# Optimization experiments

Measured on AMD Instinct MI355X. Metric: run time of the kernel, lower is better.

## Reference

```python
import jax, jax.numpy as jnp
import numpy as np
import math

B, S, E, H = 2, 2048, 1024, 16
D = E // H
EPS = 1e-5


def setup_inputs() -> dict:
    key = jax.random.key(0)
    ks = jax.random.split(key, 6)
    s = 1.0 / math.sqrt(E)
    return {
        "query": jax.random.normal(ks[0], (B, S, E), jnp.float32),
        "Wq": jax.random.normal(ks[1], (E, E), jnp.float32) * s,
        "bq": jnp.zeros((E,), jnp.float32),
        "Wk": jax.random.normal(ks[2], (E, E), jnp.float32) * s,
        "bk": jnp.zeros((E,), jnp.float32),
        "Wv": jax.random.normal(ks[3], (E, E), jnp.float32) * s,
        "bv": jnp.zeros((E,), jnp.float32),
        "Wo": jax.random.normal(ks[4], (E, E), jnp.float32) * s,
        "bo": jnp.zeros((E,), jnp.float32),
        "alpha": jnp.ones((1,), jnp.float32),
    }


def reference(query, Wq, bq, Wk, bk, Wv, bv, Wo, bo, alpha):
    # Q/K/V projections (nn.Linear: x @ W.T + b)
    q = (query @ Wq.T + bq).reshape(B, S, H, D)
    k = (query @ Wk.T + bk).reshape(B, S, H, D)
    v = (query @ Wv.T + bv).reshape(B, S, H, D)

    # YAT scores: (q.k)^2 / (||q-k||^2 + eps)
    qk = jnp.einsum('bqhd,bkhd->bhqk', q, k)          # [B,H,S,S]
    sq = jnp.einsum('bqhd,bqhd->bhq', q, q)           # ||q||^2
    sk = jnp.einsum('bkhd,bkhd->bhk', k, k)           # ||k||^2
    dist_sq = sq[..., :, None] + sk[..., None, :] - 2.0 * qk
    scores = (qk * qk) / (dist_sq + EPS)

    # learnable alpha scaling: scores * (sqrt(d)/log(1+d))^alpha
    scale = (jnp.sqrt(jnp.float32(D)) / jnp.log1p(jnp.float32(D))) ** alpha[0]
    scores = scores * scale

    attn = jax.nn.softmax(scores, axis=-1)
    out = jnp.einsum('bhqk,bkhd->bqhd', attn, v).reshape(B, S, E)
    return out @ Wo.T + bo
```

## Files before the change

kernel.cpp:

```cpp
#include <hip/hip_runtime.h>
#include <hip/hip_fp16.h>
#include <math.h>

#define BB 2
#define SS 2048
#define EE 1024
#define HH 16
#define DD 64
#define YAT_EPS 1e-5f
#define RR (BB * HH * SS)

typedef __attribute__((ext_vector_type(8))) short bf16x8;
typedef __attribute__((ext_vector_type(4))) short short4v;
typedef __attribute__((ext_vector_type(4))) float f32x4;
#define MFMA16(a, b, c) __builtin_amdgcn_mfma_f32_16x16x32_bf16((a), (b), (c), 0, 0, 0)

#if __has_builtin(__builtin_amdgcn_exp2f)
#define EXP2(x) __builtin_amdgcn_exp2f(x)
#else
#define EXP2(x) exp2f(x)
#endif
#if __has_builtin(__builtin_amdgcn_rcpf)
#define RCPF(x) __builtin_amdgcn_rcpf(x)
#else
#define RCPF(x) (1.0f / (x))
#endif

__device__ __forceinline__ unsigned short f2bf(float x) {
    unsigned int u = __float_as_uint(x);
    u += 0x7FFFu + ((u >> 16) & 1u);
    return (unsigned short)(u >> 16);
}
__device__ __forceinline__ float bf2f(unsigned short h) {
    return __uint_as_float(((unsigned int)h) << 16);
}
__device__ __forceinline__ short f2bf_t(float x) {
    return (short)(__float_as_uint(x) >> 16);
}

__device__ __forceinline__ void async_ld16(void* lds, const void* g) {
    __builtin_amdgcn_global_load_lds(
        (const __attribute__((address_space(1))) unsigned int*)g,
        (__attribute__((address_space(3))) unsigned int*)lds, 16, 0, 0);
}

__global__ __launch_bounds__(256) void split_f32(const float* __restrict__ in,
                                                 unsigned short* __restrict__ hi,
                                                 unsigned short* __restrict__ lo,
                                                 int n4) {
    int i = blockIdx.x * 256 + threadIdx.x;
    if (i >= n4) return;
    float4 v = ((const float4*)in)[i];
    ushort4 h, l;
    h.x = f2bf(v.x); l.x = f2bf(v.x - bf2f(h.x));
    h.y = f2bf(v.y); l.y = f2bf(v.y - bf2f(h.y));
    h.z = f2bf(v.z); l.z = f2bf(v.z - bf2f(h.z));
    h.w = f2bf(v.w); l.w = f2bf(v.w - bf2f(h.w));
    ((ushort4*)hi)[i] = h;
    ((ushort4*)lo)[i] = l;
}

__global__ __launch_bounds__(256) void split_w4(
        const float* __restrict__ Wq, const float* __restrict__ Wk,
        const float* __restrict__ Wv, const float* __restrict__ Wo,
        unsigned short* __restrict__ Whi, unsigned short* __restrict__ Wlo,
        unsigned short* __restrict__ Wohi) {
    int i = blockIdx.x * 256 + threadIdx.x;
    int y = blockIdx.y;
    const float* src = y == 0 ? Wq : y == 1 ? Wk : y == 2 ? Wv : Wo;
    unsigned short* hi = y < 3 ? Whi + (size_t)y * EE * EE : Wohi;
    float4 v = ((const float4*)src)[i];
    ushort4 h;
    h.x = f2bf(v.x); h.y = f2bf(v.y); h.z = f2bf(v.z); h.w = f2bf(v.w);
    ((ushort4*)hi)[i] = h;
    if (y < 2) {
        unsigned short* lo = Wlo + (size_t)y * EE * EE;
        ushort4 l;
        l.x = f2bf(v.x - bf2f(h.x));
        l.y = f2bf(v.y - bf2f(h.y));
        l.z = f2bf(v.z - bf2f(h.z));
        l.w = f2bf(v.w - bf2f(h.w));
        ((ushort4*)lo)[i] = l;
    }
}

template <int MODE, int PASSES>
__global__ __launch_bounds__(256, 2) void gemm3p(
        const unsigned short* __restrict__ Ahi, const unsigned short* __restrict__ Alo,
        const unsigned short* __restrict__ Bhi, const unsigned short* __restrict__ Blo,
        const float* __restrict__ bq, const float* __restrict__ bk,
        const float* __restrict__ bv,
        float* __restrict__ Cf,
        unsigned short* __restrict__ qhi, unsigned short* __restrict__ qlo,
        unsigned short* __restrict__ khi,
        unsigned short* __restrict__ v_sd,
        float* __restrict__ sqn, float* __restrict__ skn,
        int M, int N, int K) {
    __shared__ __align__(16) unsigned short LA_hi[128 * 32];
    __shared__ __align__(16) unsigned short LA_lo[128 * 32];
    __shared__ __align__(16) unsigned short LB_hi[128 * 32];
    __shared__ __align__(16) unsigned short LB_lo[128 * 32];

    const int t = threadIdx.x;
    const int w = t >> 6, lane = t & 63;
    const int quad = lane >> 4, lr = lane & 15;
    const int wy = w & 1, wx = w >> 1;
    const int m0 = blockIdx.y * 128, n0 = blockIdx.x * 128;

    const unsigned short* gsrc = nullptr;
    unsigned short* ldst = nullptr;
    if (w == 0)      { gsrc = Ahi + (size_t)m0 * K; ldst = LA_hi; }
    else if (w == 2) { gsrc = Bhi + (size_t)n0 * K; ldst = LB_hi; }
    else if (PASSES == 3 && w == 1) { gsrc = Alo + (size_t)m0 * K; ldst = LA_lo; }
    else if (PASSES == 3 && w == 3) { gsrc = Blo + (size_t)n0 * K; ldst = LB_lo; }
    const unsigned short* gl = gsrc ? gsrc + (size_t)(lane >> 2) * K + (lane & 3) * 8
                                    : nullptr;

    f32x4 acc[4][4];
    #pragma unroll
    for (int i = 0; i < 4; ++i)
        #pragma unroll
        for (int j = 0; j < 4; ++j)
            acc[i][j] = (f32x4){0.f, 0.f, 0.f, 0.f};

    for (int k0 = 0; k0 < K; k0 += 32) {
        __syncthreads();
        if (gl) {
            #pragma unroll
            for (int i = 0; i < 8; ++i)
                async_ld16(ldst + i * 512, gl + (size_t)i * 16 * K + k0);
        }
        __syncthreads();
        bf16x8 ah[4], al[4], bh_[4], bl_[4];
        #pragma unroll
        for (int i = 0; i < 4; ++i) {
            ah[i]  = *(const bf16x8*)&LA_hi[(wy * 64 + i * 16 + lr) * 32 + quad * 8];
            bh_[i] = *(const bf16x8*)&LB_hi[(wx * 64 + i * 16 + lr) * 32 + quad * 8];
            if (PASSES == 3) {
                al[i]  = *(const bf16x8*)&LA_lo[(wy * 64 + i * 16 + lr) * 32 + quad * 8];
                bl_[i] = *(const bf16x8*)&LB_lo[(wx * 64 + i * 16 + lr) * 32 + quad * 8];
            }
        }
        #pragma unroll
        for (int mg = 0; mg < 4; ++mg)
            #pragma unroll
            for (int ns = 0; ns < 4; ++ns) {
                f32x4 a = acc[mg][ns];
                a = MFMA16(ah[mg], bh_[ns], a);
                if (PASSES == 3) {
                    a = MFMA16(ah[mg], bl_[ns], a);
                    a = MFMA16(al[mg], bh_[ns], a);
                }
                acc[mg][ns] = a;
            }
    }

    const int ng = n0 + wx * 64;
    if (MODE == 0) {
        float bias_v[4];
        #pragma unroll
        for (int ns = 0; ns < 4; ++ns) bias_v[ns] = bq[ng + ns * 16 + lr];
        #pragma unroll
        for (int mg = 0; mg < 4; ++mg)
            #pragma unroll
            for (int r = 0; r < 4; ++r) {
                int m = m0 + wy * 64 + mg * 16 + quad * 4 + r;
                #pragma unroll
                for (int ns = 0; ns < 4; ++ns)
                    Cf[(size_t)m * N + ng + ns * 16 + lr] = acc[mg][ns][r] + bias_v[ns];
            }
    } else {
        const int path = MODE == 1 ? (ng >> 10) : 2;
        const int c = MODE == 1 ? (ng & 1023) : ng;
        const int h = c >> 6;
        const float* bias = path == 0 ? bq : path == 1 ? bk : bv;
        unsigned short* hi_p = path == 0 ? qhi : path == 1 ? khi : v_sd;
        float* nrm = path == 0 ? sqn : skn;
        float bias_v[4];
        #pragma unroll
        for (int ns = 0; ns < 4; ++ns) bias_v[ns] = bias[c + ns * 16 + lr];
        #pragma unroll
        for (int mg = 0; mg < 4; ++mg)
            #pragma unroll
            for (int r = 0; r < 4; ++r) {
                int m = m0 + wy * 64 + mg * 16 + quad * 4 + r;
                int b = m >> 11, s = m & (SS - 1);
                size_t base = ((size_t)(b * HH + h) * SS + s) * DD;
                float v4[4];
                #pragma unroll
                for (int ns = 0; ns < 4; ++ns) v4[ns] = acc[mg][ns][r] + bias_v[ns];
                if (path < 2) {
                    float pn = v4[0] * v4[0] + v4[1] * v4[1] + v4[2] * v4[2] + v4[3] * v4[3];
                    #pragma unroll
                    for (int off = 1; off < 16; off <<= 1) pn += __shfl_xor(pn, off);
                    if (lr == 0) nrm[(size_t)(b * HH + h) * SS + s] = pn;
                    #pragma unroll
                    for (int ns = 0; ns < 4; ++ns) {
                        unsigned short hv = f2bf(v4[ns]);
                        hi_p[base + ns * 16 + lr] = hv;
                        if (path == 0)
                            qlo[base + ns * 16 + lr] = f2bf(v4[ns] - bf2f(hv));
                    }
                } else {
                    #pragma unroll
                    for (int ns = 0; ns < 4; ++ns)
                        hi_p[base + ns * 16 + lr] = f2bf(v4[ns]);
                }
            }
    }
}

__global__ __launch_bounds__(256) void transpose_v(const unsigned short* __restrict__ v_sd,
                                                   unsigned short* __restrict__ vt) {
    __shared__ unsigned short T[64][65];
    const int t = threadIdx.x;
    const int bh = blockIdx.y, s0 = blockIdx.x * 64;
    {
        int sl = t >> 2, d4 = (t & 3) * 16;
        const unsigned short* src = &v_sd[((size_t)bh * SS + s0 + sl) * DD + d4];
        bf16x8 a = *(const bf16x8*)src;
        bf16x8 b = *(const bf16x8*)(src + 8);
        #pragma unroll
        for (int j = 0; j < 8; ++j) {
            T[sl][d4 + j] = (unsigned short)a[j];
            T[sl][d4 + 8 + j] = (unsigned short)b[j];
        }
    }
    __syncthreads();
    {
        int dl = t >> 2, s4 = (t & 3) * 16;
        bf16x8 a, b;
        #pragma unroll
        for (int j = 0; j < 8; ++j) {
            a[j] = (short)T[s4 + j][dl];
            b[j] = (short)T[s4 + 8 + j][dl];
        }
        unsigned short* dst = &vt[((size_t)bh * DD + dl) * SS + s0 + s4];
        *(bf16x8*)dst = a;
        *(bf16x8*)(dst + 8) = b;
    }
}

__global__ __launch_bounds__(256, 3) void yat_attn_mfma(
        const unsigned short* __restrict__ qhi, const unsigned short* __restrict__ qlo,
        const unsigned short* __restrict__ khi,
        const unsigned short* __restrict__ vt,
        const float* __restrict__ sqn, const float* __restrict__ skn,
        const float* __restrict__ alphap,
        __half* __restrict__ Opart, float2* __restrict__ mlpart) {
    __shared__ __align__(16) unsigned short Ks[2][8192];
    __shared__ __align__(16) unsigned short Ps[2][4][16 * 68];

    const int t = threadIdx.x;
    const int w = t >> 6, lane = t & 63;
    const int quad = lane >> 4, lr = lane & 15;
    const int qt = blockIdx.x, bh = blockIdx.y, z = blockIdx.z;
    const int row0 = qt * 64 + w * 16;
    const float cscale = powf(sqrtf((float)DD) / log1pf((float)DD), alphap[0])
                         * 1.4426950408889634f;

    bf16x8 qh[2], ql[2];
    #pragma unroll
    for (int kd = 0; kd < 2; ++kd) {
        size_t o = ((size_t)bh * SS + row0 + lr) * DD + kd * 32 + quad * 8;
        qh[kd] = *(const bf16x8*)&qhi[o];
        ql[kd] = *(const bf16x8*)&qlo[o];
    }
    const float sqe = sqn[(size_t)bh * SS + row0 + lr] + YAT_EPS;

    const int lrow = lane >> 3;
    const int lofs = lrow * 64 + (((lane & 7) ^ (lrow & 7)) << 3);
    const int sw = lr & 7;

    float m_r = -INFINITY, l_r = 0.f;
    f32x4 O[4];
    #pragma unroll
    for (int nd = 0; nd < 4; ++nd) O[nd] = (f32x4){0.f, 0.f, 0.f, 0.f};

    const int t0 = z * 16;
    const size_t khi_base = (size_t)bh * SS * 64 + (size_t)w * 16 * 64 + lofs;
    const size_t skn_base = (size_t)bh * SS + quad * 4;

    #pragma unroll
    for (int tl = 0; tl < 2; ++tl)
        #pragma unroll
        for (int i2 = 0; i2 < 2; ++i2)
            async_ld16(&Ks[0][tl * 4096 + w * 1024 + i2 * 512],
                       khi + khi_base + (size_t)(t0 + tl) * 4096 + i2 * 512);

    for (int it = 0; it < 8; ++it) {
        const int p = it & 1;
        __syncthreads();
        if (it + 1 < 8) {
            #pragma unroll
            for (int tl = 0; tl < 2; ++tl)
                #pragma unroll
                for (int i2 = 0; i2 < 2; ++i2)
                    async_ld16(&Ks[p ^ 1][tl * 4096 + w * 1024 + i2 * 512],
                               khi + khi_base
                                   + (size_t)(t0 + 2 * (it + 1) + tl) * 4096
                                   + i2 * 512);
        }
        #pragma unroll
        for (int sub = 0; sub < 2; ++sub) {
            const int kbase = (t0 + 2 * it + sub) * 64;
            const unsigned short* kb = &Ks[p][sub * 4096];
            f32x4 acc[4];
            f32x4 sk4[4];
            #pragma unroll
            for (int st = 0; st < 4; ++st) {
                const int rbase = (st * 16 + lr) * 64;
                bf16x8 kh0 = *(const bf16x8*)&kb[rbase + ((quad    ) ^ sw) * 8];
                bf16x8 kh1 = *(const bf16x8*)&kb[rbase + ((quad + 4) ^ sw) * 8];
                sk4[st] = *(const f32x4*)&skn[skn_base + kbase + st * 16];
                f32x4 a = (f32x4){0.f, 0.f, 0.f, 0.f};
                a = MFMA16(kh0, qh[0], a);
                a = MFMA16(kh1, qh[1], a);
                a = MFMA16(kh0, ql[0], a);
                a = MFMA16(kh1, ql[1], a);
                acc[st] = a;
            }
            bf16x8 vf[4][2];
            #pragma unroll
            for (int nd = 0; nd < 4; ++nd)
                #pragma unroll
                for (int kk = 0; kk < 2; ++kk)
                    vf[nd][kk] = *(const bf16x8*)&vt[((size_t)bh * DD + nd * 16 + lr) * SS
                                                     + kbase + kk * 32 + quad * 8];
            float mx = -INFINITY;
            #pragma unroll
            for (int st = 0; st < 4; ++st)
                #pragma unroll
                for (int r = 0; r < 4; ++r) {
                    float qk = acc[st][r];
                    float d = sqe + sk4[st][r] - 2.f * qk;
                    float u = qk * qk * RCPF(d);
                    acc[st][r] = u;
                    mx = fmaxf(mx, u);
                }
            mx = fmaxf(mx, __shfl_xor(mx, 16));
            mx = fmaxf(mx, __shfl_xor(mx, 32));
            float mnew = fmaxf(m_r, mx);
            float cm = cscale * mnew;
            float aa = EXP2(__builtin_fmaf(cscale, m_r, -cm));
            m_r = mnew;
            unsigned short* myP = Ps[p][w];
            float rs = 0.f;
            #pragma unroll
            for (int st = 0; st < 4; ++st) {
                float e0 = EXP2(__builtin_fmaf(cscale, acc[st][0], -cm));
                float e1 = EXP2(__builtin_fmaf(cscale, acc[st][1], -cm));
                float e2 = EXP2(__builtin_fmaf(cscale, acc[st][2], -cm));
                float e3 = EXP2(__builtin_fmaf(cscale, acc[st][3], -cm));
                rs += (e0 + e1) + (e2 + e3);
                short4v pv;
                pv[0] = f2bf_t(e0); pv[1] = f2bf_t(e1);
                pv[2] = f2bf_t(e2); pv[3] = f2bf_t(e3);
                *(short4v*)&myP[lr * 68 + st * 16 + quad * 4] = pv;
            }
            rs += __shfl_xor(rs, 16);
            rs += __shfl_xor(rs, 32);
            l_r = l_r * aa + rs;
            float al_[4];
            #pragma unroll
            for (int r = 0; r < 4; ++r) al_[r] = __shfl(aa, quad * 4 + r);
            #pragma unroll
            for (int nd = 0; nd < 4; ++nd)
                #pragma unroll
                for (int r = 0; r < 4; ++r)
                    O[nd][r] *= al_[r];
            bf16x8 pf[2];
            #pragma unroll
            for (int kk = 0; kk < 2; ++kk)
                pf[kk] = *(const bf16x8*)&myP[lr * 68 + kk * 32 + quad * 8];
            #pragma unroll
            for (int nd = 0; nd < 4; ++nd)
                #pragma unroll
                for (int kk = 0; kk < 2; ++kk)
                    O[nd] = MFMA16(pf[kk], vf[nd][kk], O[nd]);
        }
    }
    if (quad == 0)
        mlpart[(size_t)z * RR + (size_t)bh * SS + row0 + lr] =
            make_float2(cscale * m_r, l_r);
    #pragma unroll
    for (int r = 0; r < 4; ++r) {
        size_t rowg = (size_t)bh * SS + row0 + quad * 4 + r;
        #pragma unroll
        for (int nd = 0; nd < 4; ++nd)
            Opart[((size_t)z * RR + rowg) * DD + nd * 16 + lr] =
                __float2half(O[nd][r]);
    }
}

__global__ __launch_bounds__(256) void combine_attn(
        const __half* __restrict__ Opart, const float2* __restrict__ mlpart,
        unsigned short* __restrict__ ctxhi) {
    int tid = blockIdx.x * 256 + threadIdx.x;
    int row = tid >> 4, c4 = (tid & 15) * 4;
    float2 ml0 = mlpart[row];
    float2 ml1 = mlpart[RR + row];
    float ms = fmaxf(ml0.x, ml1.x);
    float a0 = EXP2(ml0.x - ms), a1 = EXP2(ml1.x - ms);
    float inv = RCPF(ml0.y * a0 + ml1.y * a1);
    a0 *= inv; a1 *= inv;
    const __half* p0 = Opart + (size_t)row * DD + c4;
    const __half* p1 = p0 + (size_t)RR * DD;
    int bh = row >> 11, s = row & (SS - 1);
    int b = bh >> 4, h = bh & 15;
    size_t idx = ((size_t)b * SS + s) * EE + h * DD + c4;
    ushort4 hv;
    unsigned short* hp = (unsigned short*)&hv;
    #pragma unroll
    for (int j = 0; j < 4; ++j) {
        float o = __half2float(p0[j]) * a0 + __half2float(p1[j]) * a1;
        hp[j] = f2bf(o);
    }
    *(ushort4*)&ctxhi[idx] = hv;
}

extern "C" void kernel_launch(void* const* d_in, const int* in_sizes, int n_in,
                              void* d_out, int out_size, void* d_ws, size_t ws_size,
                              hipStream_t stream) {
    const float* x     = (const float*)d_in[0];
    const float* Wq    = (const float*)d_in[1];
    const float* bq    = (const float*)d_in[2];
    const float* Wk    = (const float*)d_in[3];
    const float* bk    = (const float*)d_in[4];
    const float* Wv    = (const float*)d_in[5];
    const float* bv    = (const float*)d_in[6];
    const float* Wo    = (const float*)d_in[7];
    const float* bo    = (const float*)d_in[8];
    const float* alpha = (const float*)d_in[9];
    float* out = (float*)d_out;
    char* ws = (char*)d_ws;

    const int M = BB * SS;
    const size_t MB = 1u << 20;
    unsigned short* xhi  = (unsigned short*)(ws + 0 * MB);
    unsigned short* xlo  = (unsigned short*)(ws + 8 * MB);
    unsigned short* Whi  = (unsigned short*)(ws + 16 * MB);
    unsigned short* Wlo  = (unsigned short*)(ws + 22 * MB);
    unsigned short* vt   = (unsigned short*)(ws + 16 * MB);
    float2* mlpart       = (float2*)(ws + 24 * MB);
    unsigned short* Wohi = (unsigned short*)(ws + 28 * MB);
    unsigned short* qhi  = (unsigned short*)(ws + 32 * MB);
    unsigned short* qlo  = (unsigned short*)(ws + 40 * MB);
    unsigned short* khi  = (unsigned short*)(ws + 48 * MB);
    unsigned short* v_sd = (unsigned short*)(ws + 64 * MB);
    __half* Opart        = (__half*)(ws + 64 * MB);
    float* sqn = (float*)(ws + 80 * MB);
    float* skn = (float*)(ws + 80 * MB + 256 * 1024);
    unsigned short* ctxhi = xhi;

    const int nX = M * EE / 4, nW = EE * EE / 4;
    split_f32<<<nX / 256, 256, 0, stream>>>(x, xhi, xlo, nX);
    split_w4<<<dim3(nW / 256, 4), 256, 0, stream>>>(Wq, Wk, Wv, Wo, Whi, Wlo, Wohi);

    gemm3p<1, 3><<<dim3(2 * EE / 128, M / 128), 256, 0, stream>>>(
        xhi, xlo, Whi, Wlo, bq, bk, nullptr, nullptr,
        qhi, qlo, khi, nullptr, sqn, skn, M, 2 * EE, EE);
    gemm3p<2, 1><<<dim3(EE / 128, M / 128), 256, 0, stream>>>(
        xhi, nullptr, Whi + 2 * (size_t)EE * EE, nullptr, nullptr, nullptr, bv, nullptr,
        nullptr, nullptr, nullptr, v_sd, nullptr, nullptr, M, EE, EE);

    transpose_v<<<dim3(SS / 64, BB * HH), 256, 0, stream>>>(v_sd, vt);

    yat_attn_mfma<<<dim3(SS / 64, BB * HH, 2), 256, 0, stream>>>(
        qhi, qlo, khi, vt, sqn, skn, alpha, Opart, mlpart);

    combine_attn<<<RR * 16 / 256, 256, 0, stream>>>(Opart, mlpart, ctxhi);

    gemm3p<0, 1><<<dim3(EE / 128, M / 128), 256, 0, stream>>>(
        ctxhi, nullptr, Wohi, nullptr, bo, nullptr, nullptr, out,
        nullptr, nullptr, nullptr, nullptr, nullptr, nullptr, M, EE, EE);
}
```

Baseline: 358.8 us.

## Drop LDS K staging, read K from global, add lazy rescale and setprio

Removes the double-buffered shared-memory K tile and its per-iteration barriers. Each wave now loads K fragments straight from global memory, which frees LDS and raises the occupancy target to 4 blocks per CU. It also adds a lazy online-softmax rescale that skips the exp and accumulator rescale unless the running max grows by more than a threshold, and raises wave priority around the MFMA sections. The cost is more uncached global traffic for K and reliance on L2 hits. The threshold also lets unnormalized exponentials grow up to 2^8, which should still fit fp32 and bf16 range.

After: 451.4 us. +25.8%, slower.

```diff
diff --git a/kernel.cpp b/kernel.cpp
--- a/kernel.cpp
+++ b/kernel.cpp
@@ -241,15 +241,14 @@
     }
 }
 
-__global__ __launch_bounds__(256, 3) void yat_attn_mfma(
+__global__ __launch_bounds__(256, 4) void yat_attn_mfma(
         const unsigned short* __restrict__ qhi, const unsigned short* __restrict__ qlo,
         const unsigned short* __restrict__ khi,
         const unsigned short* __restrict__ vt,
         const float* __restrict__ sqn, const float* __restrict__ skn,
         const float* __restrict__ alphap,
         __half* __restrict__ Opart, float2* __restrict__ mlpart) {
-    __shared__ __align__(16) unsigned short Ks[2][8192];
-    __shared__ __align__(16) unsigned short Ps[2][4][16 * 68];
+    __shared__ __align__(16) unsigned short Ps[4][16 * 68];
 
     const int t = threadIdx.x;
     const int w = t >> 6, lane = t & 63;
@@ -268,99 +267,93 @@
     }
     const float sqe = sqn[(size_t)bh * SS + row0 + lr] + YAT_EPS;
 
-    const int lrow = lane >> 3;
-    const int lofs = lrow * 64 + (((lane & 7) ^ (lrow & 7)) << 3);
-    const int sw = lr & 7;
-
     float m_r = -INFINITY, l_r = 0.f;
     f32x4 O[4];
     #pragma unroll
     for (int nd = 0; nd < 4; ++nd) O[nd] = (f32x4){0.f, 0.f, 0.f, 0.f};
 
-    const int t0 = z * 16;
-    const size_t khi_base = (size_t)bh * SS * 64 + (size_t)w * 16 * 64 + lofs;
+    const size_t krow = (size_t)bh * SS;
     const size_t skn_base = (size_t)bh * SS + quad * 4;
-
-    #pragma unroll
-    for (int tl = 0; tl < 2; ++tl)
-        #pragma unroll
-        for (int i2 = 0; i2 < 2; ++i2)
-            async_ld16(&Ks[0][tl * 4096 + w * 1024 + i2 * 512],
-                       khi + khi_base + (size_t)(t0 + tl) * 4096 + i2 * 512);
-
-    for (int it = 0; it < 8; ++it) {
-        const int p = it & 1;
-        __syncthreads();
-        if (it + 1 < 8) {
-            #pragma unroll
-            for (int tl = 0; tl < 2; ++tl)
-                #pragma unroll
-                for (int i2 = 0; i2 < 2; ++i2)
-                    async_ld16(&Ks[p ^ 1][tl * 4096 + w * 1024 + i2 * 512],
-                               khi + khi_base
-                                   + (size_t)(t0 + 2 * (it + 1) + tl) * 4096
-                                   + i2 * 512);
-        }
-        #pragma unroll
-        for (int sub = 0; sub < 2; ++sub) {
-            const int kbase = (t0 + 2 * it + sub) * 64;
-            const unsigned short* kb = &Ks[p][sub * 4096];
-            f32x4 acc[4];
-            f32x4 sk4[4];
-            #pragma unroll
-            for (int st = 0; st < 4; ++st) {
-                const int rbase = (st * 16 + lr) * 64;
-                bf16x8 kh0 = *(const bf16x8*)&kb[rbase + ((quad    ) ^ sw) * 8];
-                bf16x8 kh1 = *(const bf16x8*)&kb[rbase + ((quad + 4) ^ sw) * 8];
-                sk4[st] = *(const f32x4*)&skn[skn_base + kbase + st * 16];
-                f32x4 a = (f32x4){0.f, 0.f, 0.f, 0.f};
-                a = MFMA16(kh0, qh[0], a);
-                a = MFMA16(kh1, qh[1], a);
-                a = MFMA16(kh0, ql[0], a);
-                a = MFMA16(kh1, ql[1], a);
-                acc[st] = a;
-            }
-            bf16x8 vf[4][2];
-            #pragma unroll
-            for (int nd = 0; nd < 4; ++nd)
-                #pragma unroll
-                for (int kk = 0; kk < 2; ++kk)
-                    vf[nd][kk] = *(const bf16x8*)&vt[((size_t)bh * DD + nd * 16 + lr) * SS
-                                                     + kbase + kk * 32 + quad * 8];
-            float mx = -INFINITY;
-            #pragma unroll
-            for (int st = 0; st < 4; ++st)
-                #pragma unroll
-                for (int r = 0; r < 4; ++r) {
-                    float qk = acc[st][r];
-                    float d = sqe + sk4[st][r] - 2.f * qk;
-                    float u = qk * qk * RCPF(d);
-                    acc[st][r] = u;
-                    mx = fmaxf(mx, u);
-                }
-            mx = fmaxf(mx, __shfl_xor(mx, 16));
-            mx = fmaxf(mx, __shfl_xor(mx, 32));
-            float mnew = fmaxf(m_r, mx);
-            float cm = cscale * mnew;
-            float aa = EXP2(__builtin_fmaf(cscale, m_r, -cm));
+    unsigned short* myP = Ps[w];
+
+    for (int sub = 0; sub < 16; ++sub) {
+        const int kbase = (z * 16 + sub) * 64;
+        f32x4 acc[4];
+        f32x4 sk4[4];
+        __builtin_amdgcn_s_setprio(1);
+        #pragma unroll
+        for (int st = 0; st < 4; ++st) {
+            const unsigned short* kb = &khi[(krow + kbase + st * 16 + lr) * 64];
+            bf16x8 kh0 = *(const bf16x8*)&kb[quad * 8];
+            bf16x8 kh1 = *(const bf16x8*)&kb[32 + quad * 8];
+            sk4[st] = *(const f32x4*)&skn[skn_base + kbase + st * 16];
+            f32x4 a = (f32x4){0.f, 0.f, 0.f, 0.f};
+            a = MFMA16(kh0, qh[0], a);
+            a = MFMA16(kh1, qh[1], a);
+            a = MFMA16(kh0, ql[0], a);
+            a = MFMA16(kh1, ql[1], a);
+            acc[st] = a;
+        }
+        __builtin_amdgcn_s_setprio(0);
+        bf16x8 vf[4][2];
+        #pragma unroll
+        for (int nd = 0; nd < 4; ++nd)
+            #pragma unroll
+            for (int kk = 0; kk < 2; ++kk)
+                vf[nd][kk] = *(const bf16x8*)&vt[((size_t)bh * DD + nd * 16 + lr) * SS
+                                                 + kbase + kk * 32 + quad * 8];
+        float mx = -INFINITY;
+        #pragma unroll
+        for (int st = 0; st < 4; ++st) {
+            float u0, u1, u2, u3;
+            {
+                float qk = acc[st][0];
+                u0 = qk * qk * RCPF(sqe + sk4[st][0] - 2.f * qk);
+            }
+            {
+                float qk = acc[st][1];
+                u1 = qk * qk * RCPF(sqe + sk4[st][1] - 2.f * qk);
+            }
+            {
+                float qk = acc[st][2];
+                u2 = qk * qk * RCPF(sqe + sk4[st][2] - 2.f * qk);
+            }
+            {
+                float qk = acc[st][3];
+                u3 = qk * qk * RCPF(sqe + sk4[st][3] - 2.f * qk);
+            }
+            acc[st][0] = u0; acc[st][1] = u1;
+            acc[st][2] = u2; acc[st][3] = u3;
+            mx = fmaxf(mx, fmaxf(fmaxf(u0, u1), fmaxf(u2, u3)));
+        }
+        mx = fmaxf(mx, __shfl_xor(mx, 16));
+        mx = fmaxf(mx, __shfl_xor(mx, 32));
+        float mnew = fmaxf(m_r, mx);
+        bool resc = !__all(cscale * (mnew - m_r) <= 8.f);
+        float aa = 1.f;
+        if (resc) {
+            float cmn = cscale * mnew;
+            aa = EXP2(__builtin_fmaf(cscale, m_r, -cmn));
             m_r = mnew;
-            unsigned short* myP = Ps[p][w];
-            float rs = 0.f;
-            #pragma unroll
-            for (int st = 0; st < 4; ++st) {
-                float e0 = EXP2(__builtin_fmaf(cscale, acc[st][0], -cm));
-                float e1 = EXP2(__builtin_fmaf(cscale, acc[st][1], -cm));
-                float e2 = EXP2(__builtin_fmaf(cscale, acc[st][2], -cm));
-                float e3 = EXP2(__builtin_fmaf(cscale, acc[st][3], -cm));
-                rs += (e0 + e1) + (e2 + e3);
-                short4v pv;
-                pv[0] = f2bf_t(e0); pv[1] = f2bf_t(e1);
-                pv[2] = f2bf_t(e2); pv[3] = f2bf_t(e3);
-                *(short4v*)&myP[lr * 68 + st * 16 + quad * 4] = pv;
-            }
-            rs += __shfl_xor(rs, 16);
-            rs += __shfl_xor(rs, 32);
-            l_r = l_r * aa + rs;
+        }
+        const float cm = cscale * m_r;
+        float rs = 0.f;
+        #pragma unroll
+        for (int st = 0; st < 4; ++st) {
+            float e0 = EXP2(__builtin_fmaf(cscale, acc[st][0], -cm));
+            float e1 = EXP2(__builtin_fmaf(cscale, acc[st][1], -cm));
+            float e2 = EXP2(__builtin_fmaf(cscale, acc[st][2], -cm));
+            float e3 = EXP2(__builtin_fmaf(cscale, acc[st][3], -cm));
+            rs += (e0 + e1) + (e2 + e3);
+            short4v pv;
+            pv[0] = f2bf_t(e0); pv[1] = f2bf_t(e1);
+            pv[2] = f2bf_t(e2); pv[3] = f2bf_t(e3);
+            *(short4v*)&myP[lr * 68 + st * 16 + quad * 4] = pv;
+        }
+        rs += __shfl_xor(rs, 16);
+        rs += __shfl_xor(rs, 32);
+        l_r = l_r * aa + rs;
+        if (resc) {
             float al_[4];
             #pragma unroll
             for (int r = 0; r < 4; ++r) al_[r] = __shfl(aa, quad * 4 + r);
@@ -369,16 +362,18 @@
                 #pragma unroll
                 for (int r = 0; r < 4; ++r)
                     O[nd][r] *= al_[r];
-            bf16x8 pf[2];
+        }
+        bf16x8 pf[2];
+        #pragma unroll
+        for (int kk = 0; kk < 2; ++kk)
+            pf[kk] = *(const bf16x8*)&myP[lr * 68 + kk * 32 + quad * 8];
+        __builtin_amdgcn_s_setprio(1);
+        #pragma unroll
+        for (int nd = 0; nd < 4; ++nd)
             #pragma unroll
             for (int kk = 0; kk < 2; ++kk)
-                pf[kk] = *(const bf16x8*)&myP[lr * 68 + kk * 32 + quad * 8];
-            #pragma unroll
-            for (int nd = 0; nd < 4; ++nd)
-                #pragma unroll
-                for (int kk = 0; kk < 2; ++kk)
-                    O[nd] = MFMA16(pf[kk], vf[nd][kk], O[nd]);
-        }
+                O[nd] = MFMA16(pf[kk], vf[nd][kk], O[nd]);
+        __builtin_amdgcn_s_setprio(0);
     }
     if (quad == 0)
         mlpart[(size_t)z * RR + (size_t)bh * SS + row0 + lr] =
```

## Shrink K tile staging, raise occupancy, add lazy softmax rescaling

Applied to the files above, without the earlier changes.

Each iteration now stages one 64-key tile instead of two and drops the double-buffered P scratch, roughly halving LDS per block. Launch bounds rise from 3 to 6 blocks per CU. Online softmax now rescales the running max and O accumulators only when some lane's max grows by more than a threshold, skipping most exp and multiply work. In exchange there are twice as many barriers per key range, tighter register limits that may cause spills, and a single P buffer per wave.

Measured after the change: 464.0 us. 1.29x slower.

```diff
diff --git a/kernel.cpp b/kernel.cpp
--- a/kernel.cpp
+++ b/kernel.cpp
@@ -241,15 +241,15 @@
     }
 }
 
-__global__ __launch_bounds__(256, 3) void yat_attn_mfma(
+__global__ __launch_bounds__(256, 6) void yat_attn_mfma(
         const unsigned short* __restrict__ qhi, const unsigned short* __restrict__ qlo,
         const unsigned short* __restrict__ khi,
         const unsigned short* __restrict__ vt,
         const float* __restrict__ sqn, const float* __restrict__ skn,
         const float* __restrict__ alphap,
         __half* __restrict__ Opart, float2* __restrict__ mlpart) {
-    __shared__ __align__(16) unsigned short Ks[2][8192];
-    __shared__ __align__(16) unsigned short Ps[2][4][16 * 68];
+    __shared__ __align__(16) unsigned short Ks[2][4096];
+    __shared__ __align__(16) unsigned short Ps[4][16 * 68];
 
     const int t = threadIdx.x;
     const int w = t >> 6, lane = t & 63;
@@ -280,87 +280,84 @@
     const int t0 = z * 16;
     const size_t khi_base = (size_t)bh * SS * 64 + (size_t)w * 16 * 64 + lofs;
     const size_t skn_base = (size_t)bh * SS + quad * 4;
-
-    #pragma unroll
-    for (int tl = 0; tl < 2; ++tl)
-        #pragma unroll
-        for (int i2 = 0; i2 < 2; ++i2)
-            async_ld16(&Ks[0][tl * 4096 + w * 1024 + i2 * 512],
-                       khi + khi_base + (size_t)(t0 + tl) * 4096 + i2 * 512);
-
-    for (int it = 0; it < 8; ++it) {
+    unsigned short* myP = Ps[w];
+
+    #pragma unroll
+    for (int i2 = 0; i2 < 2; ++i2)
+        async_ld16(&Ks[0][w * 1024 + i2 * 512],
+                   khi + khi_base + (size_t)t0 * 4096 + i2 * 512);
+
+    for (int it = 0; it < 16; ++it) {
         const int p = it & 1;
         __syncthreads();
-        if (it + 1 < 8) {
-            #pragma unroll
-            for (int tl = 0; tl < 2; ++tl)
-                #pragma unroll
-                for (int i2 = 0; i2 < 2; ++i2)
-                    async_ld16(&Ks[p ^ 1][tl * 4096 + w * 1024 + i2 * 512],
-                               khi + khi_base
-                                   + (size_t)(t0 + 2 * (it + 1) + tl) * 4096
-                                   + i2 * 512);
-        }
-        #pragma unroll
-        for (int sub = 0; sub < 2; ++sub) {
-            const int kbase = (t0 + 2 * it + sub) * 64;
-            const unsigned short* kb = &Ks[p][sub * 4096];
-            f32x4 acc[4];
-            f32x4 sk4[4];
-            #pragma unroll
-            for (int st = 0; st < 4; ++st) {
-                const int rbase = (st * 16 + lr) * 64;
-                bf16x8 kh0 = *(const bf16x8*)&kb[rbase + ((quad    ) ^ sw) * 8];
-                bf16x8 kh1 = *(const bf16x8*)&kb[rbase + ((quad + 4) ^ sw) * 8];
-                sk4[st] = *(const f32x4*)&skn[skn_base + kbase + st * 16];
-                f32x4 a = (f32x4){0.f, 0.f, 0.f, 0.f};
-                a = MFMA16(kh0, qh[0], a);
-                a = MFMA16(kh1, qh[1], a);
-                a = MFMA16(kh0, ql[0], a);
-                a = MFMA16(kh1, ql[1], a);
-                acc[st] = a;
+        if (it + 1 < 16) {
+            #pragma unroll
+            for (int i2 = 0; i2 < 2; ++i2)
+                async_ld16(&Ks[p ^ 1][w * 1024 + i2 * 512],
+                           khi + khi_base + (size_t)(t0 + it + 1) * 4096 + i2 * 512);
+        }
+        const int kbase = (t0 + it) * 64;
+        const unsigned short* kb = Ks[p];
+        f32x4 acc[4];
+        f32x4 sk4[4];
+        #pragma unroll
+        for (int st = 0; st < 4; ++st) {
+            const int rbase = (st * 16 + lr) * 64;
+            bf16x8 kh0 = *(const bf16x8*)&kb[rbase + ((quad    ) ^ sw) * 8];
+            bf16x8 kh1 = *(const bf16x8*)&kb[rbase + ((quad + 4) ^ sw) * 8];
+            sk4[st] = *(const f32x4*)&skn[skn_base + kbase + st * 16];
+            f32x4 a = (f32x4){0.f, 0.f, 0.f, 0.f};
+            a = MFMA16(kh0, qh[0], a);
+            a = MFMA16(kh1, qh[1], a);
+            a = MFMA16(kh0, ql[0], a);
+            a = MFMA16(kh1, ql[1], a);
+            acc[st] = a;
+        }
+        bf16x8 vf[4][2];
+        #pragma unroll
+        for (int nd = 0; nd < 4; ++nd)
+            #pragma unroll
+            for (int kk = 0; kk < 2; ++kk)
+                vf[nd][kk] = *(const bf16x8*)&vt[((size_t)bh * DD + nd * 16 + lr) * SS
+                                                 + kbase + kk * 32 + quad * 8];
+        float mx = -INFINITY;
+        #pragma unroll
+        for (int st = 0; st < 4; ++st)
+            #pragma unroll
+            for (int r = 0; r < 4; ++r) {
+                float qk = acc[st][r];
+                float d = sqe + sk4[st][r] - 2.f * qk;
+                float u = qk * qk * RCPF(d);
+                acc[st][r] = u;
+                mx = fmaxf(mx, u);
             }
-            bf16x8 vf[4][2];
-            #pragma unroll
-            for (int nd = 0; nd < 4; ++nd)
-                #pragma unroll
-                for (int kk = 0; kk < 2; ++kk)
-                    vf[nd][kk] = *(const bf16x8*)&vt[((size_t)bh * DD + nd * 16 + lr) * SS
-                                                     + kbase + kk * 32 + quad * 8];
-            float mx = -INFINITY;
-            #pragma unroll
-            for (int st = 0; st < 4; ++st)
-                #pragma unroll
-                for (int r = 0; r < 4; ++r) {
-                    float qk = acc[st][r];
-                    float d = sqe + sk4[st][r] - 2.f * qk;
-                    float u = qk * qk * RCPF(d);
-                    acc[st][r] = u;
-                    mx = fmaxf(mx, u);
-                }
-            mx = fmaxf(mx, __shfl_xor(mx, 16));
-            mx = fmaxf(mx, __shfl_xor(mx, 32));
-            float mnew = fmaxf(m_r, mx);
-            float cm = cscale * mnew;
-            float aa = EXP2(__builtin_fmaf(cscale, m_r, -cm));
+        mx = fmaxf(mx, __shfl_xor(mx, 16));
+        mx = fmaxf(mx, __shfl_xor(mx, 32));
+        float mnew = fmaxf(m_r, mx);
+        bool resc = !__all(cscale * (mnew - m_r) <= 8.f);
+        float aa = 1.f;
+        if (resc) {
+            aa = EXP2(__builtin_fmaf(cscale, m_r, -cscale * mnew));
             m_r = mnew;
-            unsigned short* myP = Ps[p][w];
-            float rs = 0.f;
-            #pragma unroll
-            for (int st = 0; st < 4; ++st) {
-                float e0 = EXP2(__builtin_fmaf(cscale, acc[st][0], -cm));
-                float e1 = EXP2(__builtin_fmaf(cscale, acc[st][1], -cm));
-                float e2 = EXP2(__builtin_fmaf(cscale, acc[st][2], -cm));
-                float e3 = EXP2(__builtin_fmaf(cscale, acc[st][3], -cm));
-                rs += (e0 + e1) + (e2 + e3);
-                short4v pv;
-                pv[0] = f2bf_t(e0); pv[1] = f2bf_t(e1);
-                pv[2] = f2bf_t(e2); pv[3] = f2bf_t(e3);
-                *(short4v*)&myP[lr * 68 + st * 16 + quad * 4] = pv;
-            }
-            rs += __shfl_xor(rs, 16);
-            rs += __shfl_xor(rs, 32);
-            l_r = l_r * aa + rs;
+        }
+        const float cm = cscale * m_r;
+        float rs = 0.f;
+        #pragma unroll
+        for (int st = 0; st < 4; ++st) {
+            float e0 = EXP2(__builtin_fmaf(cscale, acc[st][0], -cm));
+            float e1 = EXP2(__builtin_fmaf(cscale, acc[st][1], -cm));
+            float e2 = EXP2(__builtin_fmaf(cscale, acc[st][2], -cm));
+            float e3 = EXP2(__builtin_fmaf(cscale, acc[st][3], -cm));
+            rs += (e0 + e1) + (e2 + e3);
+            short4v pv;
+            pv[0] = f2bf_t(e0); pv[1] = f2bf_t(e1);
+            pv[2] = f2bf_t(e2); pv[3] = f2bf_t(e3);
+            *(short4v*)&myP[lr * 68 + st * 16 + quad * 4] = pv;
+        }
+        rs += __shfl_xor(rs, 16);
+        rs += __shfl_xor(rs, 32);
+        l_r = l_r * aa + rs;
+        if (resc) {
             float al_[4];
             #pragma unroll
             for (int r = 0; r < 4; ++r) al_[r] = __shfl(aa, quad * 4 + r);
@@ -369,16 +366,16 @@
                 #pragma unroll
                 for (int r = 0; r < 4; ++r)
                     O[nd][r] *= al_[r];
-            bf16x8 pf[2];
+        }
+        bf16x8 pf[2];
+        #pragma unroll
+        for (int kk = 0; kk < 2; ++kk)
+            pf[kk] = *(const bf16x8*)&myP[lr * 68 + kk * 32 + quad * 8];
+        #pragma unroll
+        for (int nd = 0; nd < 4; ++nd)
             #pragma unroll
             for (int kk = 0; kk < 2; ++kk)
-                pf[kk] = *(const bf16x8*)&myP[lr * 68 + kk * 32 + quad * 8];
-            #pragma unroll
-            for (int nd = 0; nd < 4; ++nd)
-                #pragma unroll
-                for (int kk = 0; kk < 2; ++kk)
-                    O[nd] = MFMA16(pf[kk], vf[nd][kk], O[nd]);
-        }
+                O[nd] = MFMA16(pf[kk], vf[nd][kk], O[nd]);
     }
     if (quad == 0)
         mlpart[(size_t)z * RR + (size_t)bh * SS + row0 + lr] =
```
